# Performance work log

Measured on AMD Instinct MI355X. Metric: run time of the kernel, lower is better.

Reference implementation:

```python
import jax, jax.numpy as jnp
import numpy as np

B, N, C = 16, 196608, 2

def setup_inputs() -> dict:
    key = jax.random.key(0)
    k1, k2, k3, k4, k5 = jax.random.split(key, 5)
    return {
        "r": jax.random.normal(k1, (B, N, C), dtype=jnp.float32),
        "w": jax.random.uniform(k2, (B, N, 2), dtype=jnp.float32),
        "J_p": jax.random.normal(k3, (B, N, C, 6), dtype=jnp.float32),
        "J_d": jax.random.uniform(k4, (B, N, C, 1), dtype=jnp.float32),
        "lmbda": jax.random.uniform(k5, (B, 1, 1), dtype=jnp.float32),
    }

def reference(r, w, J_p, J_d, lmbda):
    # r: (B,N,C)  w: (B,N,2)  J_p: (B,N,C,6)  J_d: (B,N,C,1)  lmbda: (B,1,1)
    conf = w[..., 0:1]                                  # (B,N,1)
    node_lambda = w[..., 1:2]                           # (B,N,1)
    conf4 = conf[..., None]                             # (B,N,1,1)
    Jd = J_d[..., 0]                                    # (B,N,C)

    # Gauss-Newton blocks (sum-over-N reductions of tiny outer products)
    H_pp = jnp.einsum('bnki,bnkj->bij', J_p, conf4 * J_p)        # (B,6,6)
    H_pd = jnp.einsum('bnki,bnkj->bnij', J_p, conf4 * J_d)       # (B,N,6,1)
    H_dd = jnp.einsum('bnk,bnk->bn', Jd, conf * Jd)[..., None]   # (B,N,1)
    wr = conf * r                                                # (B,N,C)
    g_p = jnp.einsum('bnki,bnk->bi', J_p, wr)[..., None]         # (B,6,1)
    g_d = jnp.einsum('bnk,bnk->bn', Jd, wr)[..., None]           # (B,N,1)

    eye6 = jnp.eye(6, dtype=H_pp.dtype)[None]                    # (1,6,6)
    H_pp = H_pp + lmbda * eye6                                   # LM damping on pose block

    # Depth block damping + safe inverse
    H_dd_safe = jnp.maximum(H_dd + lmbda + node_lambda, 1e-4)    # (B,N,1)
    inv_H_dd = 1.0 / H_dd_safe                                   # (B,N,1)

    # Schur complement: H_eff = H_pp - sum_n H_pd invHdd H_pd^T
    H_pd_invHdd = H_pd * inv_H_dd[..., None]                     # (B,N,6,1)
    term = jnp.einsum('bnik,bnjk->bij', H_pd_invHdd, H_pd)       # (B,6,6)
    H_eff = H_pp - term + (0.01 + 0.001) * eye6                  # eye*0.01 then ridge 0.001
    g_eff = g_p - jnp.sum(H_pd_invHdd * g_d[..., None], axis=1)  # (B,6,1)

    delta_pose = jnp.linalg.solve(H_eff, g_eff)                  # (B,6,1)
    dp = delta_pose[..., 0]                                      # (B,6)

    # Back-substitute depths
    v = jnp.einsum('bnij,bi->bnj', H_pd, dp)                     # (B,N,1)
    delta_depth = inv_H_dd * (g_d - v)                           # (B,N,1)

    delta_pose_out = jnp.clip(dp, -2.0, 2.0)                     # (B,6)
    return (delta_pose_out, delta_depth)
```

## Files before the change

### kernel.cpp

```cpp
#include <hip/hip_runtime.h>


constexpr int NACC = 27;

__device__ __forceinline__ void accum_point(
    float ja0, float ja1, float ja2, float ja3, float ja4, float ja5,
    float jb0, float jb1, float jb2, float jb3, float jb4, float jb5,
    float r0, float r1, float conf, float nlam, float jd0, float jd1,
    float lam, float* __restrict__ A, float* __restrict__ g)
{
    const float ja[6] = {ja0, ja1, ja2, ja3, ja4, ja5};
    const float jb[6] = {jb0, jb1, jb2, jb3, jb4, jb5};
    float h[6], gp[6];
#pragma unroll
    for (int i = 0; i < 6; ++i) {
        h[i]  = conf * (ja[i] * jd0 + jb[i] * jd1);
        gp[i] = conf * (ja[i] * r0 + jb[i] * r1);
    }
    const float hdd = conf * (jd0 * jd0 + jd1 * jd1);
    const float inv = 1.0f / fmaxf(hdd + lam + nlam, 1e-4f);
    const float gd  = conf * (jd0 * r0 + jd1 * r1);
    const float gdinv = gd * inv;
    int idx = 0;
#pragma unroll
    for (int i = 0; i < 6; ++i) {
        const float hii = h[i] * inv;
#pragma unroll
        for (int j = i; j < 6; ++j) {
            A[idx] += conf * (ja[i] * ja[j] + jb[i] * jb[j]) - hii * h[j];
            ++idx;
        }
        g[i] += gp[i] - h[i] * gdinv;
    }
}

__global__ __launch_bounds__(256) void dba_reduce(
    const float* __restrict__ r, const float* __restrict__ w,
    const float* __restrict__ J_p, const float* __restrict__ J_d,
    const float* __restrict__ lmbda, float* __restrict__ acc, int N)
{
    const int b = blockIdx.y;
    const float lam = lmbda[b];
    float A[21];
    float g[6];
#pragma unroll
    for (int i = 0; i < 21; ++i) A[i] = 0.f;
#pragma unroll
    for (int i = 0; i < 6; ++i) g[i] = 0.f;

    const size_t base = (size_t)b * (size_t)N;
    const int P = N >> 1;
    const int stride = gridDim.x * blockDim.x;
    for (int pr = blockIdx.x * blockDim.x + threadIdx.x; pr < P; pr += stride) {
        const size_t p = base + (size_t)(pr << 1);
        const float4 rv = *(const float4*)(r + p * 2);
        const float4 wv = *(const float4*)(w + p * 2);
        const float4 jd = *(const float4*)(J_d + p * 2);
        const float4* jp = (const float4*)(J_p + p * 12);
        const float4 q0 = jp[0];
        const float4 q1 = jp[1];
        const float4 q2 = jp[2];
        const float4 q3 = jp[3];
        const float4 q4 = jp[4];
        const float4 q5 = jp[5];

        accum_point(q0.x, q0.y, q0.z, q0.w, q1.x, q1.y,
                    q1.z, q1.w, q2.x, q2.y, q2.z, q2.w,
                    rv.x, rv.y, wv.x, wv.y, jd.x, jd.y, lam, A, g);
        accum_point(q3.x, q3.y, q3.z, q3.w, q4.x, q4.y,
                    q4.z, q4.w, q5.x, q5.y, q5.z, q5.w,
                    rv.z, rv.w, wv.z, wv.w, jd.z, jd.w, lam, A, g);
    }

    float v[NACC];
#pragma unroll
    for (int i = 0; i < 21; ++i) v[i] = A[i];
#pragma unroll
    for (int i = 0; i < 6; ++i) v[21 + i] = g[i];

#pragma unroll
    for (int off = 32; off > 0; off >>= 1) {
#pragma unroll
        for (int i = 0; i < NACC; ++i) v[i] += __shfl_down(v[i], off, 64);
    }

    __shared__ float sred[4][NACC];
    const int wave = threadIdx.x >> 6;
    const int lane = threadIdx.x & 63;
    if (lane == 0) {
#pragma unroll
        for (int i = 0; i < NACC; ++i) sred[wave][i] = v[i];
    }
    __syncthreads();
    if (threadIdx.x < NACC) {
        const float s = sred[0][threadIdx.x] + sred[1][threadIdx.x] +
                        sred[2][threadIdx.x] + sred[3][threadIdx.x];
        atomicAdd(&acc[b * 32 + threadIdx.x], s);
    }
}

__global__ void dba_solve(const float* __restrict__ acc,
                          const float* __restrict__ lmbda,
                          float* __restrict__ pose_out,
                          float* __restrict__ dp_ws, int B)
{
    const int b = blockIdx.x * blockDim.x + threadIdx.x;
    if (b >= B) return;
    float M[6][7];
    const float* a = acc + b * 32;
    int idx = 0;
#pragma unroll
    for (int i = 0; i < 6; ++i) {
#pragma unroll
        for (int j = i; j < 6; ++j) {
            const float t = a[idx++];
            M[i][j] = t;
            M[j][i] = t;
        }
    }
#pragma unroll
    for (int i = 0; i < 6; ++i) M[i][6] = a[21 + i];
    const float lam = lmbda[b];
#pragma unroll
    for (int i = 0; i < 6; ++i) M[i][i] += lam + 0.011f;

#pragma unroll
    for (int k = 0; k < 6; ++k) {
        const float piv = 1.0f / M[k][k];
#pragma unroll
        for (int j = 0; j < 7; ++j) M[k][j] *= piv;
#pragma unroll
        for (int i = 0; i < 6; ++i) {
            if (i == k) continue;
            const float f = M[i][k];
#pragma unroll
            for (int j = 0; j < 7; ++j) M[i][j] -= f * M[k][j];
        }
    }
#pragma unroll
    for (int i = 0; i < 6; ++i) {
        const float x = M[i][6];
        dp_ws[b * 6 + i] = x;
        pose_out[b * 6 + i] = fminf(fmaxf(x, -2.0f), 2.0f);
    }
}

__global__ __launch_bounds__(256) void dba_depth(
    const float* __restrict__ r, const float* __restrict__ w,
    const float* __restrict__ J_p, const float* __restrict__ J_d,
    const float* __restrict__ lmbda, const float* __restrict__ dp_ws,
    float* __restrict__ depth_out, int N)
{
    const int b = blockIdx.y;
    const float lam = lmbda[b];
    float dp[6];
#pragma unroll
    for (int i = 0; i < 6; ++i) dp[i] = dp_ws[b * 6 + i];

    const size_t base = (size_t)b * (size_t)N;
    const int P = N >> 1;
    const int stride = gridDim.x * blockDim.x;
    for (int pr = blockIdx.x * blockDim.x + threadIdx.x; pr < P; pr += stride) {
        const size_t p = base + (size_t)(pr << 1);
        const float4 rv = *(const float4*)(r + p * 2);
        const float4 wv = *(const float4*)(w + p * 2);
        const float4 jd = *(const float4*)(J_d + p * 2);
        const float4* jp = (const float4*)(J_p + p * 12);
        const float4 q0 = jp[0];
        const float4 q1 = jp[1];
        const float4 q2 = jp[2];
        const float4 q3 = jp[3];
        const float4 q4 = jp[4];
        const float4 q5 = jp[5];

        float2 outv;
        {
            const float ja[6] = {q0.x, q0.y, q0.z, q0.w, q1.x, q1.y};
            const float jb[6] = {q1.z, q1.w, q2.x, q2.y, q2.z, q2.w};
            float v = 0.f;
#pragma unroll
            for (int i = 0; i < 6; ++i)
                v += (ja[i] * jd.x + jb[i] * jd.y) * dp[i];
            v *= wv.x;
            const float hdd = wv.x * (jd.x * jd.x + jd.y * jd.y);
            const float inv = 1.0f / fmaxf(hdd + lam + wv.y, 1e-4f);
            const float gd  = wv.x * (jd.x * rv.x + jd.y * rv.y);
            outv.x = inv * (gd - v);
        }
        {
            const float ja[6] = {q3.x, q3.y, q3.z, q3.w, q4.x, q4.y};
            const float jb[6] = {q4.z, q4.w, q5.x, q5.y, q5.z, q5.w};
            float v = 0.f;
#pragma unroll
            for (int i = 0; i < 6; ++i)
                v += (ja[i] * jd.z + jb[i] * jd.w) * dp[i];
            v *= wv.z;
            const float hdd = wv.z * (jd.z * jd.z + jd.w * jd.w);
            const float inv = 1.0f / fmaxf(hdd + lam + wv.w, 1e-4f);
            const float gd  = wv.z * (jd.z * rv.z + jd.w * rv.w);
            outv.y = inv * (gd - v);
        }
        *(float2*)(depth_out + p) = outv;
    }
}

extern "C" void kernel_launch(void* const* d_in, const int* in_sizes, int n_in,
                              void* d_out, int out_size, void* d_ws, size_t ws_size,
                              hipStream_t stream)
{
    const float* r   = (const float*)d_in[0];
    const float* w   = (const float*)d_in[1];
    const float* J_p = (const float*)d_in[2];
    const float* J_d = (const float*)d_in[3];
    const float* lmb = (const float*)d_in[4];
    const int B = in_sizes[4];
    const int N = in_sizes[0] / (B * 2);

    float* acc   = (float*)d_ws;
    float* dp_ws = (float*)d_ws + B * 32;
    float* out   = (float*)d_out;

    hipMemsetAsync(acc, 0, B * 32 * sizeof(float), stream);

    dim3 grid(192, B);
    dba_reduce<<<grid, 256, 0, stream>>>(r, w, J_p, J_d, lmb, acc, N);
    dba_solve<<<1, 64, 0, stream>>>(acc, lmb, out, dp_ws, B);
    dba_depth<<<grid, 256, 0, stream>>>(r, w, J_p, J_d, lmb, dp_ws, out + B * 6, N);
}
```

Baseline: 306.4 us.

## Stage J_p through per-wave LDS tiles for coalesced loads in both kernels

Both the reduce and depth kernels now load each wave's 128-point slice of J_p as contiguous float4s, one per lane, and scatter the values into a padded per-wave shared-memory tile. Each lane then reads its own 24 Jacobian values back out of that tile. The goal is to replace the old 48-byte-strided per-thread loads with fully coalesced wave-wide loads. The grid is also halved to 96 blocks per batch to match the 512-point tiling. In exchange this adds LDS traffic, 25 KB of shared memory per block and fewer resident blocks. It also relies on N being a multiple of 512 and on intra-wave LDS ordering without a barrier.

```diff
diff --git a/kernel.cpp b/kernel.cpp
--- a/kernel.cpp
+++ b/kernel.cpp
@@ -4,13 +4,10 @@
 constexpr int NACC = 27;
 
 __device__ __forceinline__ void accum_point(
-    float ja0, float ja1, float ja2, float ja3, float ja4, float ja5,
-    float jb0, float jb1, float jb2, float jb3, float jb4, float jb5,
+    const float* __restrict__ ja, const float* __restrict__ jb,
     float r0, float r1, float conf, float nlam, float jd0, float jd1,
     float lam, float* __restrict__ A, float* __restrict__ g)
 {
-    const float ja[6] = {ja0, ja1, ja2, ja3, ja4, ja5};
-    const float jb[6] = {jb0, jb1, jb2, jb3, jb4, jb5};
     float h[6], gp[6];
 #pragma unroll
     for (int i = 0; i < 6; ++i) {
@@ -34,42 +31,61 @@
     }
 }
 
+__device__ __forceinline__ void stage_jp(
+    const float* __restrict__ J_p, size_t wp, int lane,
+    float (*__restrict__ ldsw)[65])
+{
+    const float4* jp4 = (const float4*)(J_p + wp * 12);
+#pragma unroll
+    for (int q = 0; q < 6; ++q) {
+        const int l4 = (q << 6) + lane;
+        const float4 v = jp4[l4];
+        const int pair = l4 / 6;
+        const int s4 = l4 - 6 * pair;
+        ldsw[4 * s4 + 0][pair] = v.x;
+        ldsw[4 * s4 + 1][pair] = v.y;
+        ldsw[4 * s4 + 2][pair] = v.z;
+        ldsw[4 * s4 + 3][pair] = v.w;
+    }
+}
+
 __global__ __launch_bounds__(256) void dba_reduce(
     const float* __restrict__ r, const float* __restrict__ w,
     const float* __restrict__ J_p, const float* __restrict__ J_d,
     const float* __restrict__ lmbda, float* __restrict__ acc, int N)
 {
+    __shared__ float lds[4][24][65];
+    __shared__ float sred[4][NACC];
     const int b = blockIdx.y;
     const float lam = lmbda[b];
-    float A[21];
-    float g[6];
+    const int wave = threadIdx.x >> 6;
+    const int lane = threadIdx.x & 63;
+
+    float A[21], g[6];
 #pragma unroll
     for (int i = 0; i < 21; ++i) A[i] = 0.f;
 #pragma unroll
     for (int i = 0; i < 6; ++i) g[i] = 0.f;
 
     const size_t base = (size_t)b * (size_t)N;
-    const int P = N >> 1;
-    const int stride = gridDim.x * blockDim.x;
-    for (int pr = blockIdx.x * blockDim.x + threadIdx.x; pr < P; pr += stride) {
-        const size_t p = base + (size_t)(pr << 1);
+    const int tiles = N >> 9;
+    for (int tile = blockIdx.x; tile < tiles; tile += gridDim.x) {
+        const size_t wp = base + ((size_t)tile << 9) + (wave << 7);
+        stage_jp(J_p, wp, lane, lds[wave]);
+
+        const size_t p = wp + (lane << 1);
         const float4 rv = *(const float4*)(r + p * 2);
         const float4 wv = *(const float4*)(w + p * 2);
         const float4 jd = *(const float4*)(J_d + p * 2);
-        const float4* jp = (const float4*)(J_p + p * 12);
-        const float4 q0 = jp[0];
-        const float4 q1 = jp[1];
-        const float4 q2 = jp[2];
-        const float4 q3 = jp[3];
-        const float4 q4 = jp[4];
-        const float4 q5 = jp[5];
-
-        accum_point(q0.x, q0.y, q0.z, q0.w, q1.x, q1.y,
-                    q1.z, q1.w, q2.x, q2.y, q2.z, q2.w,
-                    rv.x, rv.y, wv.x, wv.y, jd.x, jd.y, lam, A, g);
-        accum_point(q3.x, q3.y, q3.z, q3.w, q4.x, q4.y,
-                    q4.z, q4.w, q5.x, q5.y, q5.z, q5.w,
-                    rv.z, rv.w, wv.z, wv.w, jd.z, jd.w, lam, A, g);
+
+        float f0[12], f1[12];
+#pragma unroll
+        for (int i = 0; i < 12; ++i) f0[i] = lds[wave][i][lane];
+#pragma unroll
+        for (int i = 0; i < 12; ++i) f1[i] = lds[wave][12 + i][lane];
+
+        accum_point(f0, f0 + 6, rv.x, rv.y, wv.x, wv.y, jd.x, jd.y, lam, A, g);
+        accum_point(f1, f1 + 6, rv.z, rv.w, wv.z, wv.w, jd.z, jd.w, lam, A, g);
     }
 
     float v[NACC];
@@ -77,16 +93,11 @@
     for (int i = 0; i < 21; ++i) v[i] = A[i];
 #pragma unroll
     for (int i = 0; i < 6; ++i) v[21 + i] = g[i];
-
 #pragma unroll
     for (int off = 32; off > 0; off >>= 1) {
 #pragma unroll
         for (int i = 0; i < NACC; ++i) v[i] += __shfl_down(v[i], off, 64);
     }
-
-    __shared__ float sred[4][NACC];
-    const int wave = threadIdx.x >> 6;
-    const int lane = threadIdx.x & 63;
     if (lane == 0) {
 #pragma unroll
         for (int i = 0; i < NACC; ++i) sred[wave][i] = v[i];
@@ -151,36 +162,38 @@
     const float* __restrict__ lmbda, const float* __restrict__ dp_ws,
     float* __restrict__ depth_out, int N)
 {
+    __shared__ float lds[4][24][65];
     const int b = blockIdx.y;
     const float lam = lmbda[b];
     float dp[6];
 #pragma unroll
     for (int i = 0; i < 6; ++i) dp[i] = dp_ws[b * 6 + i];
 
+    const int wave = threadIdx.x >> 6;
+    const int lane = threadIdx.x & 63;
     const size_t base = (size_t)b * (size_t)N;
-    const int P = N >> 1;
-    const int stride = gridDim.x * blockDim.x;
-    for (int pr = blockIdx.x * blockDim.x + threadIdx.x; pr < P; pr += stride) {
-        const size_t p = base + (size_t)(pr << 1);
+    const int tiles = N >> 9;
+    for (int tile = blockIdx.x; tile < tiles; tile += gridDim.x) {
+        const size_t wp = base + ((size_t)tile << 9) + (wave << 7);
+        stage_jp(J_p, wp, lane, lds[wave]);
+
+        const size_t p = wp + (lane << 1);
         const float4 rv = *(const float4*)(r + p * 2);
         const float4 wv = *(const float4*)(w + p * 2);
         const float4 jd = *(const float4*)(J_d + p * 2);
-        const float4* jp = (const float4*)(J_p + p * 12);
-        const float4 q0 = jp[0];
-        const float4 q1 = jp[1];
-        const float4 q2 = jp[2];
-        const float4 q3 = jp[3];
-        const float4 q4 = jp[4];
-        const float4 q5 = jp[5];
+
+        float f0[12], f1[12];
+#pragma unroll
+        for (int i = 0; i < 12; ++i) f0[i] = lds[wave][i][lane];
+#pragma unroll
+        for (int i = 0; i < 12; ++i) f1[i] = lds[wave][12 + i][lane];
 
         float2 outv;
         {
-            const float ja[6] = {q0.x, q0.y, q0.z, q0.w, q1.x, q1.y};
-            const float jb[6] = {q1.z, q1.w, q2.x, q2.y, q2.z, q2.w};
             float v = 0.f;
 #pragma unroll
             for (int i = 0; i < 6; ++i)
-                v += (ja[i] * jd.x + jb[i] * jd.y) * dp[i];
+                v += (f0[i] * jd.x + f0[6 + i] * jd.y) * dp[i];
             v *= wv.x;
             const float hdd = wv.x * (jd.x * jd.x + jd.y * jd.y);
             const float inv = 1.0f / fmaxf(hdd + lam + wv.y, 1e-4f);
@@ -188,12 +201,10 @@
             outv.x = inv * (gd - v);
         }
         {
-            const float ja[6] = {q3.x, q3.y, q3.z, q3.w, q4.x, q4.y};
-            const float jb[6] = {q4.z, q4.w, q5.x, q5.y, q5.z, q5.w};
             float v = 0.f;
 #pragma unroll
             for (int i = 0; i < 6; ++i)
-                v += (ja[i] * jd.z + jb[i] * jd.w) * dp[i];
+                v += (f1[i] * jd.z + f1[6 + i] * jd.w) * dp[i];
             v *= wv.z;
             const float hdd = wv.z * (jd.z * jd.z + jd.w * jd.w);
             const float inv = 1.0f / fmaxf(hdd + lam + wv.w, 1e-4f);
@@ -222,7 +233,7 @@
 
     hipMemsetAsync(acc, 0, B * 32 * sizeof(float), stream);
 
-    dim3 grid(192, B);
+    dim3 grid(96, B);
     dba_reduce<<<grid, 256, 0, stream>>>(r, w, J_p, J_d, lmb, acc, N);
     dba_solve<<<1, 64, 0, stream>>>(acc, lmb, out, dp_ws, B);
     dba_depth<<<grid, 256, 0, stream>>>(r, w, J_p, J_d, lmb, dp_ws, out + B * 6, N);
```

Result: no change. 311.8 us (+1.7%).

## Stash per-point Schur terms in reduce pass to shrink depth back-substitution reads

Applied to the files above, without the earlier changes.

The reduce kernel now writes, for each point, gd*inv and the six H_pd*inv coefficients to a workspace stash. The depth kernel then reads only these 32 bytes per point instead of re-reading r, w, J_p and J_d (72 bytes) and recomputing them. Input loads and stash stores use nontemporal hints. In exchange the reduce pass adds a large write stream, which may also evict input data that the second pass could otherwise have found in the last-level cache. The path runs only when the workspace is big enough; otherwise the original two-pass direct path is kept.

```diff
diff --git a/kernel.cpp b/kernel.cpp
--- a/kernel.cpp
+++ b/kernel.cpp
@@ -1,16 +1,18 @@
 #include <hip/hip_runtime.h>
 
 
+typedef float fv4 __attribute__((ext_vector_type(4)));
+typedef float fv2 __attribute__((ext_vector_type(2)));
+
 constexpr int NACC = 27;
 
-__device__ __forceinline__ void accum_point(
-    float ja0, float ja1, float ja2, float ja3, float ja4, float ja5,
-    float jb0, float jb1, float jb2, float jb3, float jb4, float jb5,
+template <bool STASH>
+__device__ __forceinline__ void accum_point_stash(
+    const float* __restrict__ ja, const float* __restrict__ jb,
     float r0, float r1, float conf, float nlam, float jd0, float jd1,
-    float lam, float* __restrict__ A, float* __restrict__ g)
-{
-    const float ja[6] = {ja0, ja1, ja2, ja3, ja4, ja5};
-    const float jb[6] = {jb0, jb1, jb2, jb3, jb4, jb5};
+    float lam, float* __restrict__ A, float* __restrict__ g,
+    fv4* __restrict__ st)
+{
     float h[6], gp[6];
 #pragma unroll
     for (int i = 0; i < 6; ++i) {
@@ -21,28 +23,35 @@
     const float inv = 1.0f / fmaxf(hdd + lam + nlam, 1e-4f);
     const float gd  = conf * (jd0 * r0 + jd1 * r1);
     const float gdinv = gd * inv;
+    float sv[6];
+#pragma unroll
+    for (int i = 0; i < 6; ++i) sv[i] = h[i] * inv;
+    if (STASH) {
+        st[0] = (fv4){gdinv, sv[0], sv[1], sv[2]};
+        st[1] = (fv4){sv[3], sv[4], sv[5], 0.f};
+    }
     int idx = 0;
 #pragma unroll
     for (int i = 0; i < 6; ++i) {
-        const float hii = h[i] * inv;
 #pragma unroll
         for (int j = i; j < 6; ++j) {
-            A[idx] += conf * (ja[i] * ja[j] + jb[i] * jb[j]) - hii * h[j];
+            A[idx] += conf * (ja[i] * ja[j] + jb[i] * jb[j]) - sv[i] * h[j];
             ++idx;
         }
         g[i] += gp[i] - h[i] * gdinv;
     }
 }
 
-__global__ __launch_bounds__(256) void dba_reduce(
+template <bool STASH>
+__global__ __launch_bounds__(256) void dba_reduce_k(
     const float* __restrict__ r, const float* __restrict__ w,
     const float* __restrict__ J_p, const float* __restrict__ J_d,
-    const float* __restrict__ lmbda, float* __restrict__ acc, int N)
+    const float* __restrict__ lmbda, float* __restrict__ acc,
+    float* __restrict__ stash, int N)
 {
     const int b = blockIdx.y;
     const float lam = lmbda[b];
-    float A[21];
-    float g[6];
+    float A[21], g[6];
 #pragma unroll
     for (int i = 0; i < 21; ++i) A[i] = 0.f;
 #pragma unroll
@@ -53,23 +62,37 @@
     const int stride = gridDim.x * blockDim.x;
     for (int pr = blockIdx.x * blockDim.x + threadIdx.x; pr < P; pr += stride) {
         const size_t p = base + (size_t)(pr << 1);
-        const float4 rv = *(const float4*)(r + p * 2);
-        const float4 wv = *(const float4*)(w + p * 2);
-        const float4 jd = *(const float4*)(J_d + p * 2);
-        const float4* jp = (const float4*)(J_p + p * 12);
-        const float4 q0 = jp[0];
-        const float4 q1 = jp[1];
-        const float4 q2 = jp[2];
-        const float4 q3 = jp[3];
-        const float4 q4 = jp[4];
-        const float4 q5 = jp[5];
-
-        accum_point(q0.x, q0.y, q0.z, q0.w, q1.x, q1.y,
-                    q1.z, q1.w, q2.x, q2.y, q2.z, q2.w,
-                    rv.x, rv.y, wv.x, wv.y, jd.x, jd.y, lam, A, g);
-        accum_point(q3.x, q3.y, q3.z, q3.w, q4.x, q4.y,
-                    q4.z, q4.w, q5.x, q5.y, q5.z, q5.w,
-                    rv.z, rv.w, wv.z, wv.w, jd.z, jd.w, lam, A, g);
+        const fv4 rv = __builtin_nontemporal_load((const fv4*)(r + p * 2));
+        const fv4 wv = __builtin_nontemporal_load((const fv4*)(w + p * 2));
+        const fv4 jd = __builtin_nontemporal_load((const fv4*)(J_d + p * 2));
+        const fv4* jp = (const fv4*)(J_p + p * 12);
+        const fv4 q0 = __builtin_nontemporal_load(jp + 0);
+        const fv4 q1 = __builtin_nontemporal_load(jp + 1);
+        const fv4 q2 = __builtin_nontemporal_load(jp + 2);
+        const fv4 q3 = __builtin_nontemporal_load(jp + 3);
+        const fv4 q4 = __builtin_nontemporal_load(jp + 4);
+        const fv4 q5 = __builtin_nontemporal_load(jp + 5);
+
+        fv4 st[4];
+        {
+            const float ja[6] = {q0.x, q0.y, q0.z, q0.w, q1.x, q1.y};
+            const float jb[6] = {q1.z, q1.w, q2.x, q2.y, q2.z, q2.w};
+            accum_point_stash<STASH>(ja, jb, rv.x, rv.y, wv.x, wv.y,
+                                     jd.x, jd.y, lam, A, g, st);
+        }
+        {
+            const float ja[6] = {q3.x, q3.y, q3.z, q3.w, q4.x, q4.y};
+            const float jb[6] = {q4.z, q4.w, q5.x, q5.y, q5.z, q5.w};
+            accum_point_stash<STASH>(ja, jb, rv.z, rv.w, wv.z, wv.w,
+                                     jd.z, jd.w, lam, A, g, st + 2);
+        }
+        if (STASH) {
+            fv4* sp = (fv4*)(stash + p * 8);
+            __builtin_nontemporal_store(st[0], sp + 0);
+            __builtin_nontemporal_store(st[1], sp + 1);
+            __builtin_nontemporal_store(st[2], sp + 2);
+            __builtin_nontemporal_store(st[3], sp + 3);
+        }
     }
 
     float v[NACC];
@@ -77,13 +100,11 @@
     for (int i = 0; i < 21; ++i) v[i] = A[i];
 #pragma unroll
     for (int i = 0; i < 6; ++i) v[21 + i] = g[i];
-
 #pragma unroll
     for (int off = 32; off > 0; off >>= 1) {
 #pragma unroll
         for (int i = 0; i < NACC; ++i) v[i] += __shfl_down(v[i], off, 64);
     }
-
     __shared__ float sred[4][NACC];
     const int wave = threadIdx.x >> 6;
     const int lane = threadIdx.x & 63;
@@ -145,14 +166,11 @@
     }
 }
 
-__global__ __launch_bounds__(256) void dba_depth(
-    const float* __restrict__ r, const float* __restrict__ w,
-    const float* __restrict__ J_p, const float* __restrict__ J_d,
-    const float* __restrict__ lmbda, const float* __restrict__ dp_ws,
+__global__ __launch_bounds__(256) void dba_depth_stash(
+    const float* __restrict__ stash, const float* __restrict__ dp_ws,
     float* __restrict__ depth_out, int N)
 {
     const int b = blockIdx.y;
-    const float lam = lmbda[b];
     float dp[6];
 #pragma unroll
     for (int i = 0; i < 6; ++i) dp[i] = dp_ws[b * 6 + i];
@@ -162,18 +180,48 @@
     const int stride = gridDim.x * blockDim.x;
     for (int pr = blockIdx.x * blockDim.x + threadIdx.x; pr < P; pr += stride) {
         const size_t p = base + (size_t)(pr << 1);
-        const float4 rv = *(const float4*)(r + p * 2);
-        const float4 wv = *(const float4*)(w + p * 2);
-        const float4 jd = *(const float4*)(J_d + p * 2);
-        const float4* jp = (const float4*)(J_p + p * 12);
-        const float4 q0 = jp[0];
-        const float4 q1 = jp[1];
-        const float4 q2 = jp[2];
-        const float4 q3 = jp[3];
-        const float4 q4 = jp[4];
-        const float4 q5 = jp[5];
-
-        float2 outv;
+        const fv4* sp = (const fv4*)(stash + p * 8);
+        const fv4 a0 = sp[0];
+        const fv4 a1 = sp[1];
+        const fv4 a2 = sp[2];
+        const fv4 a3 = sp[3];
+        fv2 outv;
+        outv.x = a0.x - (a0.y * dp[0] + a0.z * dp[1] + a0.w * dp[2] +
+                         a1.x * dp[3] + a1.y * dp[4] + a1.z * dp[5]);
+        outv.y = a2.x - (a2.y * dp[0] + a2.z * dp[1] + a2.w * dp[2] +
+                         a3.x * dp[3] + a3.y * dp[4] + a3.z * dp[5]);
+        __builtin_nontemporal_store(outv, (fv2*)(depth_out + p));
+    }
+}
+
+__global__ __launch_bounds__(256) void dba_depth_direct(
+    const float* __restrict__ r, const float* __restrict__ w,
+    const float* __restrict__ J_p, const float* __restrict__ J_d,
+    const float* __restrict__ lmbda, const float* __restrict__ dp_ws,
+    float* __restrict__ depth_out, int N)
+{
+    const int b = blockIdx.y;
+    const float lam = lmbda[b];
+    float dp[6];
+#pragma unroll
+    for (int i = 0; i < 6; ++i) dp[i] = dp_ws[b * 6 + i];
+
+    const size_t base = (size_t)b * (size_t)N;
+    const int P = N >> 1;
+    const int stride = gridDim.x * blockDim.x;
+    for (int pr = blockIdx.x * blockDim.x + threadIdx.x; pr < P; pr += stride) {
+        const size_t p = base + (size_t)(pr << 1);
+        const fv4 rv = *(const fv4*)(r + p * 2);
+        const fv4 wv = *(const fv4*)(w + p * 2);
+        const fv4 jd = *(const fv4*)(J_d + p * 2);
+        const fv4* jp = (const fv4*)(J_p + p * 12);
+        const fv4 q0 = jp[0];
+        const fv4 q1 = jp[1];
+        const fv4 q2 = jp[2];
+        const fv4 q3 = jp[3];
+        const fv4 q4 = jp[4];
+        const fv4 q5 = jp[5];
+        fv2 outv;
         {
             const float ja[6] = {q0.x, q0.y, q0.z, q0.w, q1.x, q1.y};
             const float jb[6] = {q1.z, q1.w, q2.x, q2.y, q2.z, q2.w};
@@ -200,7 +248,7 @@
             const float gd  = wv.z * (jd.z * rv.z + jd.w * rv.w);
             outv.y = inv * (gd - v);
         }
-        *(float2*)(depth_out + p) = outv;
+        *(fv2*)(depth_out + p) = outv;
     }
 }
 
@@ -218,12 +266,25 @@
 
     float* acc   = (float*)d_ws;
     float* dp_ws = (float*)d_ws + B * 32;
+    float* stash = (float*)d_ws + 1024;
     float* out   = (float*)d_out;
 
+    const size_t stash_bytes = (size_t)B * (size_t)N * 8 * sizeof(float);
+    const bool use_stash = ws_size >= 4096 + stash_bytes;
+
     hipMemsetAsync(acc, 0, B * 32 * sizeof(float), stream);
 
     dim3 grid(192, B);
-    dba_reduce<<<grid, 256, 0, stream>>>(r, w, J_p, J_d, lmb, acc, N);
-    dba_solve<<<1, 64, 0, stream>>>(acc, lmb, out, dp_ws, B);
-    dba_depth<<<grid, 256, 0, stream>>>(r, w, J_p, J_d, lmb, dp_ws, out + B * 6, N);
-}
+    if (use_stash) {
+        dba_reduce_k<true><<<grid, 256, 0, stream>>>(r, w, J_p, J_d, lmb, acc,
+                                                     stash, N);
+        dba_solve<<<1, 64, 0, stream>>>(acc, lmb, out, dp_ws, B);
+        dba_depth_stash<<<grid, 256, 0, stream>>>(stash, dp_ws, out + B * 6, N);
+    } else {
+        dba_reduce_k<false><<<grid, 256, 0, stream>>>(r, w, J_p, J_d, lmb, acc,
+                                                      nullptr, N);
+        dba_solve<<<1, 64, 0, stream>>>(acc, lmb, out, dp_ws, B);
+        dba_depth_direct<<<grid, 256, 0, stream>>>(r, w, J_p, J_d, lmb, dp_ws,
+                                                   out + B * 6, N);
+    }
+}
```

Measured after the change: 404.2 us. 31.9% more time.
